# Performance work log

Measured on AMD Instinct MI355X. Metric: run time of the kernel, lower is better.

Reference implementation:

```python
import jax, jax.numpy as jnp
import numpy as np

N_HEAD, N_KV, HEAD_DIM, GATE_CH = 16, 4, 128, 32

def _rope(x, cos, sin):
    d = x.shape[3] // 2
    x1, x2 = x[..., :d], x[..., d:]
    return jnp.concatenate([x1 * cos + x2 * sin, x1 * (-sin) + x2 * cos], axis=3)

def _rmsnorm(x):
    xf = x.astype(jnp.float32)
    return (x * jax.lax.rsqrt(jnp.mean(xf * xf, axis=-1, keepdims=True) + 1e-6)).astype(x.dtype)

def setup_inputs() -> dict:
    key = jax.random.key(0)
    ks = jax.random.split(key, 9)
    B, T, C = 2, 2048, 2048
    return {
        "x":  jax.random.normal(ks[0], (B, T, C), jnp.float32),
        "ve": jax.random.normal(ks[1], (B, T, N_KV * HEAD_DIM), jnp.float32),
        "cos": jax.random.uniform(ks[2], (T, 1, HEAD_DIM // 2), jnp.float32),
        "sin": jax.random.uniform(ks[3], (T, 1, HEAD_DIM // 2), jnp.float32),
        "Wq": jax.random.normal(ks[4], (C, N_HEAD * HEAD_DIM), jnp.float32) * 0.02,
        "Wk": jax.random.normal(ks[5], (C, N_KV * HEAD_DIM), jnp.float32) * 0.02,
        "Wv": jax.random.normal(ks[6], (C, N_KV * HEAD_DIM), jnp.float32) * 0.02,
        "Wg": jax.random.normal(ks[7], (GATE_CH, N_KV), jnp.float32) * 0.02,
        "Wo": jax.random.normal(ks[8], (C, C), jnp.float32) * 0.02,
        "window": 1024,
    }

def reference(x, ve, cos, sin, Wq, Wk, Wv, Wg, Wo, window):
    B, T, C = x.shape
    q = (x @ Wq).reshape(B, T, N_HEAD, HEAD_DIM)
    k = (x @ Wk).reshape(B, T, N_KV, HEAD_DIM)
    v = (x @ Wv).reshape(B, T, N_KV, HEAD_DIM)
    # value-embedding gate (ve_gate active for this layer)
    gate = 2.0 * jax.nn.sigmoid(x[..., :GATE_CH] @ Wg)  # (B,T,N_KV)
    v = v + gate[..., None] * ve.reshape(B, T, N_KV, HEAD_DIM)
    q, k = _rope(q, cos, sin), _rope(k, cos, sin)
    q, k = _rmsnorm(q), _rmsnorm(k)
    # GQA: repeat kv heads (repeat_interleave over head dim)
    groups = N_HEAD // N_KV
    k = jnp.repeat(k, groups, axis=2)
    v = jnp.repeat(v, groups, axis=2)
    scale = 1.0 / np.sqrt(HEAD_DIM)
    scores = jnp.einsum("bthd,bshd->bhts", q, k) * scale  # (B,H,T,T)
    idx = jnp.arange(T)
    diff = idx[None, :] - idx[:, None]  # diff[i,j] = j - i, as in torch code
    mask = (diff >= 0) & (diff < window)
    scores = jnp.where(mask[None, None], scores, -jnp.inf)
    p = jax.nn.softmax(scores, axis=-1)
    y = jnp.einsum("bhts,bshd->bthd", p, v).reshape(B, T, C)
    return y @ Wo
```

## Files before the change

kernel.cpp:

```cpp
#include <hip/hip_runtime.h>
#include <hip/hip_bf16.h>
#include <cstdint>

typedef __hip_bfloat16 bf16;
typedef __attribute__((ext_vector_type(8))) short short8;
typedef __attribute__((ext_vector_type(4))) short short4v;
typedef __attribute__((ext_vector_type(4))) float f32x4;

#define T_   2048
#define CDIM 2048
#define NH   16
#define NKV  4
#define HD   128
#define QSCALE (0.08838834764831845f * 1.44269504088896340f)

__device__ __forceinline__ void gload_lds16(const void* g, void* l) {
  __builtin_amdgcn_global_load_lds(
      (const __attribute__((address_space(1))) void*)g,
      (__attribute__((address_space(3))) void*)l, 16, 0, 0);
}

__global__ __launch_bounds__(256) void cast_x_kernel(const float4* __restrict__ in,
                                                     ushort4* __restrict__ out, int n4) {
  int i = blockIdx.x * 256 + threadIdx.x;
  if (i >= n4) return;
  float4 v = in[i];
  union { bf16 h[4]; ushort4 u; } cv;
  cv.h[0] = __float2bfloat16(v.x);
  cv.h[1] = __float2bfloat16(v.y);
  cv.h[2] = __float2bfloat16(v.z);
  cv.h[3] = __float2bfloat16(v.w);
  out[i] = cv.u;
}

__global__ __launch_bounds__(256) void cast_transpose(const float* __restrict__ W,
                                                      bf16* __restrict__ WT,
                                                      int K, int N) {
  __shared__ float tile[32][33];
  int k0 = blockIdx.y * 32, n0 = blockIdx.x * 32;
  int r = threadIdx.x >> 5, c = threadIdx.x & 31;
  for (int i = 0; i < 4; ++i)
    tile[r + i * 8][c] = W[(size_t)(k0 + r + i * 8) * N + n0 + c];
  __syncthreads();
  for (int i = 0; i < 4; ++i)
    WT[(size_t)(n0 + r + i * 8) * K + k0 + c] = __float2bfloat16(tile[c][r + i * 8]);
}

__global__ __launch_bounds__(512, 2) void gemm_qkv8(const bf16* __restrict__ A,
                                                    const bf16* __restrict__ BT,
                                                    bf16* __restrict__ C,
                                                    int N, int K, int RY, int RX) {
  __shared__ __align__(16) bf16 sA[2][256 * 64];
  __shared__ __align__(16) bf16 sB[2][256 * 64];

  int tid = threadIdx.x;
  int lane = tid & 63, w = tid >> 6;
  int wm = w >> 2, wn = w & 3;
  int lr = lane & 15, lk = lane >> 4;

  int xcd = blockIdx.x & 7, t = blockIdx.x >> 3;
  int by = (xcd >> 1) * RY + t / RX;
  int bx = (xcd & 1) * RX + t % RX;
  int m0 = by * 256, n0 = bx * 256;

  f32x4 acc[8][4];
#pragma unroll
  for (int m = 0; m < 8; ++m)
#pragma unroll
    for (int n = 0; n < 4; ++n) acc[m][n] = (f32x4){0.f, 0.f, 0.f, 0.f};

  const bf16* Abase = A + (size_t)m0 * K;
  const bf16* Bbase = BT + (size_t)n0 * K;

  auto stageB = [&](int p, int kt) {
    int kb = kt << 6;
#pragma unroll
    for (int i = 0; i < 4; ++i) {
      int c = i * 512 + tid;
      int r = c >> 3, sl = c & 7;
      gload_lds16(Bbase + (size_t)r * K + kb + ((sl ^ (r & 7)) << 3),
                  (char*)(&sB[p][0]) + c * 16);
    }
  };
  auto stageAq = [&](int p, int kt, int q) {
    int kb = kt << 6;
    int rbase = 32 * q + ((w & 3) << 3) + ((w >> 2) << 7);
    int r = rbase + (lane >> 3), sl = lane & 7;
    gload_lds16(Abase + (size_t)r * K + kb + ((sl ^ (r & 7)) << 3),
                (char*)(&sA[p][0]) + rbase * 128 + lane * 16);
  };

  int nk = K >> 6;
  stageB(0, 0);
  stageAq(0, 0, 0); stageAq(0, 0, 1); stageAq(0, 0, 2); stageAq(0, 0, 3);
  stageB(1, 1);
  stageAq(1, 1, 0); stageAq(1, 1, 1); stageAq(1, 1, 2);
  asm volatile("s_waitcnt vmcnt(7)" ::: "memory");
  __builtin_amdgcn_s_barrier();

#define READ_A(Q)                                                          \
  {                                                                        \
    _Pragma("unroll")                                                      \
    for (int mi = 0; mi < 2; ++mi) {                                       \
      int row = wm * 128 + (2 * (Q) + mi) * 16 + lr;                       \
      const char* rb = sAb + row * 128;                                    \
      int rx = (row & 7) << 4;                                             \
      af[mi][0] = *(const short8*)(rb + ((lk * 16) ^ rx));                 \
      af[mi][1] = *(const short8*)(rb + ((64 + lk * 16) ^ rx));            \
    }                                                                      \
  }
#define MFMA_Q(Q)                                                          \
  __builtin_amdgcn_s_setprio(1);                                          \
  _Pragma("unroll")                                                        \
  for (int kk = 0; kk < 2; ++kk)                                           \
    _Pragma("unroll")                                                      \
    for (int mi = 0; mi < 2; ++mi)                                         \
      _Pragma("unroll")                                                    \
      for (int n = 0; n < 4; ++n)                                          \
        acc[2 * (Q) + mi][n] = __builtin_amdgcn_mfma_f32_16x16x32_bf16(    \
            af[mi][kk], bfr[n][kk], acc[2 * (Q) + mi][n], 0, 0, 0);        \
  __builtin_amdgcn_s_setprio(0);
#define LGKM_FENCE                                                         \
  asm volatile("s_waitcnt lgkmcnt(0)" ::: "memory");                       \
  __builtin_amdgcn_sched_barrier(0);

  for (int kt = 0; kt < nk; ++kt) {
    int p = kt & 1;
    const char* sAb = (const char*)(&sA[p][0]);
    const char* sBb = (const char*)(&sB[p][0]);
    short8 bfr[4][2], af[2][2];

#pragma unroll
    for (int n = 0; n < 4; ++n) {
      int row = wn * 64 + n * 16 + lr;
      const char* rb = sBb + row * 128;
      int rx = (row & 7) << 4;
      bfr[n][0] = *(const short8*)(rb + ((lk * 16) ^ rx));
      bfr[n][1] = *(const short8*)(rb + ((64 + lk * 16) ^ rx));
    }
    READ_A(0);
    if (kt + 1 < nk) stageAq(p ^ 1, kt + 1, 3);
    LGKM_FENCE;
    MFMA_Q(0);
    __builtin_amdgcn_s_barrier();

    READ_A(1);
    if (kt + 2 < nk) { stageB(p, kt + 2); stageAq(p, kt + 2, 0); }
    LGKM_FENCE;
    MFMA_Q(1);
    __builtin_amdgcn_s_barrier();

    READ_A(2);
    if (kt + 2 < nk) stageAq(p, kt + 2, 1);
    LGKM_FENCE;
    MFMA_Q(2);
    __builtin_amdgcn_s_barrier();

    READ_A(3);
    if (kt + 2 < nk) stageAq(p, kt + 2, 2);
    LGKM_FENCE;
    MFMA_Q(3);
    if (kt + 2 < nk)
      asm volatile("s_waitcnt vmcnt(7)" ::: "memory");
    else
      asm volatile("s_waitcnt vmcnt(0)" ::: "memory");
    __builtin_amdgcn_s_barrier();
  }
#undef READ_A
#undef MFMA_Q
#undef LGKM_FENCE

#pragma unroll
  for (int m = 0; m < 8; ++m)
#pragma unroll
    for (int n = 0; n < 4; ++n)
#pragma unroll
      for (int jj = 0; jj < 4; ++jj)
        C[(size_t)(m0 + wm * 128 + m * 16 + lk * 4 + jj) * N +
          n0 + wn * 64 + n * 16 + lr] = __float2bfloat16(acc[m][n][jj]);
}

template <int MREP, typename CT>
__global__ __launch_bounds__(512, 2) void gemm_8p(const bf16* __restrict__ A,
                                                  const bf16* __restrict__ BT,
                                                  CT* __restrict__ C,
                                                  int N, int K, int RY, int RX) {
  constexpr int BM = MREP * 32;
  constexpr int ALOADS = BM / 64;
  __shared__ __align__(16) bf16 sA[2][BM * 64];
  __shared__ __align__(16) bf16 sB[2][256 * 64];

  int tid = threadIdx.x;
  int lane = tid & 63, w = tid >> 6;
  int wm = w >> 2, wn = w & 3;
  int lr = lane & 15, lk = lane >> 4;

  int xcd = blockIdx.x & 7, t = blockIdx.x >> 3;
  int by = (xcd >> 1) * RY + t / RX;
  int bx = (xcd & 1) * RX + t % RX;
  int m0 = by * BM, n0 = bx * 256;

  f32x4 acc[MREP][4];
#pragma unroll
  for (int m = 0; m < MREP; ++m)
#pragma unroll
    for (int n = 0; n < 4; ++n) acc[m][n] = (f32x4){0.f, 0.f, 0.f, 0.f};

  const bf16* Abase = A + (size_t)m0 * K;
  const bf16* Bbase = BT + (size_t)n0 * K;

  auto stage = [&](int b, int kt) {
    int kb = kt << 6;
#pragma unroll
    for (int i = 0; i < ALOADS; ++i) {
      int c = i * 512 + tid;
      int r = c >> 3, sl = c & 7;
      gload_lds16(Abase + (size_t)r * K + kb + ((sl ^ (r & 7)) << 3),
                  (char*)(&sA[b][0]) + c * 16);
    }
#pragma unroll
    for (int i = 0; i < 4; ++i) {
      int c = i * 512 + tid;
      int r = c >> 3, sl = c & 7;
      gload_lds16(Bbase + (size_t)r * K + kb + ((sl ^ (r & 7)) << 3),
                  (char*)(&sB[b][0]) + c * 16);
    }
  };

  int nk = K >> 6;
  stage(0, 0);
  stage(1, 1);
  asm volatile("s_waitcnt vmcnt(6)" ::: "memory");
  __builtin_amdgcn_s_barrier();

  for (int kt = 0; kt < nk; ++kt) {
    int d = kt & 1;
    const char* sAb = (const char*)(&sA[d][0]);
    const char* sBb = (const char*)(&sB[d][0]);

    short8 bfr[4][2];
#pragma unroll
    for (int n = 0; n < 4; ++n) {
      int row = wn * 64 + n * 16 + lr;
      const char* rb = sBb + row * 128;
      int rx = (row & 7) << 4;
      bfr[n][0] = *(const short8*)(rb + ((lk * 16) ^ rx));
      bfr[n][1] = *(const short8*)(rb + ((64 + lk * 16) ^ rx));
    }

#pragma unroll
    for (int p = 0; p < MREP / 2; ++p) {
      short8 af[2][2];
#pragma unroll
      for (int mi = 0; mi < 2; ++mi) {
        int row = wm * (MREP * 16) + (p * 2 + mi) * 16 + lr;
        const char* rb = sAb + row * 128;
        int rx = (row & 7) << 4;
        af[mi][0] = *(const short8*)(rb + ((lk * 16) ^ rx));
        af[mi][1] = *(const short8*)(rb + ((64 + lk * 16) ^ rx));
      }
      __builtin_amdgcn_s_setprio(1);
#pragma unroll
      for (int kk = 0; kk < 2; ++kk)
#pragma unroll
        for (int mi = 0; mi < 2; ++mi)
#pragma unroll
          for (int n = 0; n < 4; ++n)
            acc[p * 2 + mi][n] = __builtin_amdgcn_mfma_f32_16x16x32_bf16(
                af[mi][kk], bfr[n][kk], acc[p * 2 + mi][n], 0, 0, 0);
      __builtin_amdgcn_s_setprio(0);
    }

    asm volatile("s_waitcnt lgkmcnt(0)\n\ts_barrier" ::: "memory");
    if (kt + 2 < nk) {
      stage(d, kt + 2);
      asm volatile("s_waitcnt vmcnt(6)\n\ts_barrier" ::: "memory");
    } else {
      asm volatile("s_waitcnt vmcnt(0)\n\ts_barrier" ::: "memory");
    }
  }

#pragma unroll
  for (int m = 0; m < MREP; ++m)
#pragma unroll
    for (int n = 0; n < 4; ++n)
#pragma unroll
      for (int jj = 0; jj < 4; ++jj) {
        size_t idx = (size_t)(m0 + wm * (MREP * 16) + m * 16 + lk * 4 + jj) * N +
                     n0 + wn * 64 + n * 16 + lr;
        if constexpr (__is_same(CT, float))
          C[idx] = acc[m][n][jj];
        else
          C[idx] = __float2bfloat16(acc[m][n][jj]);
      }
}

__global__ __launch_bounds__(256) void epilogue_kernel(
    const bf16* __restrict__ qkv, const float* __restrict__ x,
    const float* __restrict__ ve, const float* __restrict__ cosT,
    const float* __restrict__ sinT, const float* __restrict__ Wg,
    bf16* __restrict__ qn, bf16* __restrict__ kn, bf16* __restrict__ vT) {
  int row = blockIdx.x;
  int bi = row >> 11, t = row & 2047;
  int tid = threadIdx.x, lane = tid & 63, w = tid >> 6;
  __shared__ float gate[NKV];
  size_t rb = (size_t)row * 3072;

  if (tid < 128) {
    int g = tid >> 5, i = tid & 31;
    float p = x[(size_t)row * CDIM + i] * Wg[i * 4 + g];
    p += __shfl_xor(p, 1);  p += __shfl_xor(p, 2);
    p += __shfl_xor(p, 4);  p += __shfl_xor(p, 8);
    p += __shfl_xor(p, 16);
    if (i == 0) gate[g] = 2.f / (1.f + __expf(-p));
  }
  __syncthreads();

  float cv = cosT[t * 64 + lane];
  float sv = sinT[t * 64 + lane];

  for (int it = 0; it < 4; ++it) {
    int h = it * 4 + w;
    float x1 = __bfloat162float(qkv[rb + h * 128 + lane]);
    float x2 = __bfloat162float(qkv[rb + h * 128 + 64 + lane]);
    float y1 = x1 * cv + x2 * sv;
    float y2 = x2 * cv - x1 * sv;
    float ss = y1 * y1 + y2 * y2;
    ss += __shfl_xor(ss, 1);  ss += __shfl_xor(ss, 2);  ss += __shfl_xor(ss, 4);
    ss += __shfl_xor(ss, 8);  ss += __shfl_xor(ss, 16); ss += __shfl_xor(ss, 32);
    float r = rsqrtf(ss * (1.f / 128.f) + 1e-6f) * QSCALE;
    size_t ob = (size_t)row * (NH * HD) + h * 128;
    qn[ob + lane] = __float2bfloat16(y1 * r);
    qn[ob + 64 + lane] = __float2bfloat16(y2 * r);
  }
  {
    int h = w;
    float x1 = __bfloat162float(qkv[rb + 2048 + h * 128 + lane]);
    float x2 = __bfloat162float(qkv[rb + 2048 + h * 128 + 64 + lane]);
    float y1 = x1 * cv + x2 * sv;
    float y2 = x2 * cv - x1 * sv;
    float ss = y1 * y1 + y2 * y2;
    ss += __shfl_xor(ss, 1);  ss += __shfl_xor(ss, 2);  ss += __shfl_xor(ss, 4);
    ss += __shfl_xor(ss, 8);  ss += __shfl_xor(ss, 16); ss += __shfl_xor(ss, 32);
    float r = rsqrtf(ss * (1.f / 128.f) + 1e-6f);
    size_t ob = (size_t)row * (NKV * HD) + h * 128;
    kn[ob + lane] = __float2bfloat16(y1 * r);
    kn[ob + 64 + lane] = __float2bfloat16(y2 * r);
  }
  for (int e = tid; e < 512; e += 256) {
    int kv = e >> 7, d = e & 127;
    float val = __bfloat162float(qkv[rb + 2560 + e]) + gate[kv] * ve[(size_t)row * 512 + e];
    vT[((size_t)(bi * NKV + kv) * HD + d) * T_ + t] = __float2bfloat16(val);
  }
}

__global__ __launch_bounds__(256, 3) void attn_kernel(
    const bf16* __restrict__ qn, const bf16* __restrict__ kn,
    const bf16* __restrict__ vT, bf16* __restrict__ y,
    const int* __restrict__ winp) {
  __shared__ __align__(16) bf16 sK[64 * 128];
  __shared__ __align__(16) bf16 sV[128 * 64];

  int win = *winp;
  int id = blockIdx.x;
  int g  = id & 7;
  int bi = g >> 2, kvh = g & 3;
  int rem = id >> 3;
  int h  = kvh * 4 + (rem & 3);
  int jslot = (rem >> 2) & 7;
  int s5 = rem >> 5;
  int q0i = (s5 == 0) ? (2 * jslot) : (s5 == 1) ? (2 * jslot + 1)
          : (s5 == 2) ? (16 + jslot) : (31 - jslot);
  int q0 = q0i << 6;
  int tid = threadIdx.x;
  int lane = tid & 63, w = tid >> 6;
  int lr = lane & 15, lk = lane >> 4;

  short8 qf[4];
  {
    const bf16* qrow = qn + (size_t)(bi * T_ + q0 + w * 16 + lr) * (NH * HD) + h * HD;
#pragma unroll
    for (int c = 0; c < 4; ++c) qf[c] = *(const short8*)(qrow + c * 32 + lk * 8);
  }

  int kge[4], klb[4], vge[4], vlbA[4], vlbB[4];
#pragma unroll
  for (int i = 0; i < 4; ++i) {
    int c = i * 256 + tid;
    int kr = c >> 4, ks = c & 15;
    kge[i] = kr * (NKV * HD) + ks * 8;
    klb[i] = kr * 256 + ((ks ^ (kr & 7)) << 4);
    int vr = c >> 3, vs = c & 7;
    vge[i] = vr * T_ + vs * 8;
    int hh = vs >> 2, m = vs & 3, a = m >> 1;
    int sA = 8 * ((2 * m) & 3) + 4 * a;
    int sB = 8 * ((2 * m + 1) & 3) + 4 * a;
    int tA = 64 * hh + 2 * sA, tB = 64 * hh + 2 * sB;
    vlbA[i] = vr * 128 + (((tA >> 4) ^ (vr & 7)) << 4) + (tA & 15);
    vlbB[i] = vr * 128 + (((tB >> 4) ^ (vr & 7)) << 4) + (tB & 15);
  }
  const bf16* kpane = kn + (size_t)bi * T_ * (NKV * HD) + kvh * HD;
  const bf16* vpane = vT + (size_t)(bi * NKV + kvh) * HD * T_;

  short8 kreg[4], vreg[4];
  auto LOAD = [&](int jtx) {
    const bf16* kb = kpane + (size_t)(jtx << 6) * (NKV * HD);
    const bf16* vb = vpane + (jtx << 6);
#pragma unroll
    for (int i = 0; i < 4; ++i) kreg[i] = *(const short8*)(kb + kge[i]);
#pragma unroll
    for (int i = 0; i < 4; ++i) vreg[i] = *(const short8*)(vb + vge[i]);
  };
  auto WRITE = [&]() {
#pragma unroll
    for (int i = 0; i < 4; ++i) *(short8*)((char*)sK + klb[i]) = kreg[i];
#pragma unroll
    for (int i = 0; i < 4; ++i) {
      union { short8 s8; short4v s4[2]; } u;
      u.s8 = vreg[i];
      *(short4v*)((char*)sV + vlbA[i]) = u.s4[0];
      *(short4v*)((char*)sV + vlbB[i]) = u.s4[1];
    }
  };

  f32x4 o[8];
#pragma unroll
  for (int i = 0; i < 8; ++i) o[i] = (f32x4){0.f, 0.f, 0.f, 0.f};
  float lpart = 0.f;

  int jt0 = q0 >> 6;
  int hi = q0 + 62 + win; if (hi > T_ - 1) hi = T_ - 1;
  int jt1 = hi >> 6;

  LOAD(jt0);
  WRITE();
  if (jt0 < jt1) LOAD(jt0 + 1);
  asm volatile("s_waitcnt lgkmcnt(0)\n\ts_barrier" ::: "memory");

  int irow = q0 + w * 16 + lr;
  int klo = lk * 4;

  for (int jt = jt0; jt <= jt1; ++jt) {
    int j0 = jt << 6;

    f32x4 s[4];
#pragma unroll
    for (int sub = 0; sub < 4; ++sub) s[sub] = (f32x4){0.f, 0.f, 0.f, 0.f};
    __builtin_amdgcn_s_setprio(1);
#pragma unroll
    for (int sub = 0; sub < 4; ++sub) {
      int kr = sub * 16 + lr;
      int rx = (kr & 7) << 4;
      const char* rowb = (const char*)sK + kr * 256;
#pragma unroll
      for (int c = 0; c < 4; ++c) {
        short8 kf = *(const short8*)(rowb + ((c * 64 + lk * 16) ^ rx));
        s[sub] = __builtin_amdgcn_mfma_f32_16x16x32_bf16(kf, qf[c], s[sub], 0, 0, 0);
      }
    }
    __builtin_amdgcn_s_setprio(0);

    bool full = (j0 >= q0 + 64) && (j0 + 64 <= q0 + win);
    int koff = j0 - irow;

    unsigned pk[8];
#pragma unroll
    for (int sub = 0; sub < 4; ++sub) {
      float p0 = exp2f(s[sub][0]), p1 = exp2f(s[sub][1]);
      float p2 = exp2f(s[sub][2]), p3 = exp2f(s[sub][3]);
      if (!full) {
        int base = koff + sub * 16 + klo;
        p0 = ((unsigned)(base + 0) < (unsigned)win) ? p0 : 0.f;
        p1 = ((unsigned)(base + 1) < (unsigned)win) ? p1 : 0.f;
        p2 = ((unsigned)(base + 2) < (unsigned)win) ? p2 : 0.f;
        p3 = ((unsigned)(base + 3) < (unsigned)win) ? p3 : 0.f;
      }
      lpart += (p0 + p1) + (p2 + p3);
      asm("v_cvt_pk_bf16_f32 %0, %1, %2" : "=v"(pk[sub * 2])     : "v"(p0), "v"(p1));
      asm("v_cvt_pk_bf16_f32 %0, %1, %2" : "=v"(pk[sub * 2 + 1]) : "v"(p2), "v"(p3));
    }
    union { unsigned u[4]; short8 s8; } c0, c1;
    c0.u[0] = pk[0]; c0.u[1] = pk[1]; c0.u[2] = pk[2]; c0.u[3] = pk[3];
    c1.u[0] = pk[4]; c1.u[1] = pk[5]; c1.u[2] = pk[6]; c1.u[3] = pk[7];
    short8 pf0 = c0.s8, pf1 = c1.s8;

    __builtin_amdgcn_s_setprio(1);
#pragma unroll
    for (int nb = 0; nb < 8; ++nb) {
      int vr = nb * 16 + lr;
      int vrx = (vr & 7) << 4;
      const char* vb = (const char*)sV + vr * 128;
      short8 vf0 = *(const short8*)(vb + ((lk * 16) ^ vrx));
      short8 vf1 = *(const short8*)(vb + ((64 + lk * 16) ^ vrx));
      o[nb] = __builtin_amdgcn_mfma_f32_16x16x32_bf16(pf0, vf0, o[nb], 0, 0, 0);
      o[nb] = __builtin_amdgcn_mfma_f32_16x16x32_bf16(pf1, vf1, o[nb], 0, 0, 0);
    }
    __builtin_amdgcn_s_setprio(0);

    asm volatile("s_waitcnt lgkmcnt(0)\n\ts_barrier" ::: "memory");
    if (jt < jt1) {
      WRITE();
      if (jt + 1 < jt1) LOAD(jt + 2);
      asm volatile("s_waitcnt lgkmcnt(0)\n\ts_barrier" ::: "memory");
    }
  }

  float l = lpart;
  l += __shfl_xor(l, 16);
  l += __shfl_xor(l, 32);
#pragma unroll
  for (int jj = 0; jj < 4; ++jj) {
    float inv = 1.f / __shfl(l, klo + jj);
    size_t ob = (size_t)(bi * T_ + q0 + w * 16 + klo + jj) * (NH * HD) + h * HD;
#pragma unroll
    for (int nb = 0; nb < 8; ++nb)
      y[ob + nb * 16 + lr] = __float2bfloat16(o[nb][jj] * inv);
  }
}

extern "C" void kernel_launch(void* const* d_in, const int* in_sizes, int n_in,
                              void* d_out, int out_size, void* d_ws, size_t ws_size,
                              hipStream_t stream) {
  const float* x    = (const float*)d_in[0];
  const float* ve   = (const float*)d_in[1];
  const float* cosT = (const float*)d_in[2];
  const float* sinT = (const float*)d_in[3];
  const float* Wq   = (const float*)d_in[4];
  const float* Wk   = (const float*)d_in[5];
  const float* Wv   = (const float*)d_in[6];
  const float* Wg   = (const float*)d_in[7];
  const float* Wo   = (const float*)d_in[8];
  const int*   win  = (const int*)d_in[9];
  float* out = (float*)d_out;

  char* ws = (char*)d_ws;
  bf16*  xb   = (bf16*)(ws);
  bf16*  wT   = (bf16*)(ws + 16777216);
  bf16*  woT  = (bf16*)(ws + 29360128);
  bf16*  qkvb = (bf16*)(ws + 37748736);
  bf16*  qn   = (bf16*)(ws + 62914560);
  bf16*  kn   = (bf16*)(ws + 79691776);
  bf16*  vTb  = (bf16*)(ws + 83886080);
  bf16*  y    = qkvb;

  cast_x_kernel<<<8192, 256, 0, stream>>>((const float4*)x, (ushort4*)xb, 2097152);
  cast_transpose<<<dim3(64, 64), 256, 0, stream>>>(Wq, wT, 2048, 2048);
  cast_transpose<<<dim3(16, 64), 256, 0, stream>>>(Wk, wT + (size_t)2048 * 2048, 2048, 512);
  cast_transpose<<<dim3(16, 64), 256, 0, stream>>>(Wv, wT + (size_t)2560 * 2048, 2048, 512);
  cast_transpose<<<dim3(64, 64), 256, 0, stream>>>(Wo, woT, 2048, 2048);

  gemm_qkv8<<<192, 512, 0, stream>>>(xb, wT, qkvb, 3072, 2048, 4, 6);
  epilogue_kernel<<<4096, 256, 0, stream>>>(qkvb, x, ve, cosT, sinT, Wg, qn, kn, vTb);
  attn_kernel<<<1024, 256, 0, stream>>>(qn, kn, vTb, y, win);
  gemm_8p<4, float><<<256, 512, 0, stream>>>(y, woT, out, 2048, 2048, 8, 4);
}
```

Before: 200.9 us.

## Unify GEMMs into phased template; retile QKV GEMM to fill all CUs

Replaces the two GEMM kernels with one template, gemm_pp, parameterized by M and N repeat counts. It uses the phased pipeline in which A-tile loads are interleaved across four MFMA phases. The QKV projection now uses 256x192 tiles, giving a 256-block grid instead of 192 blocks, so every CU gets work. The output projection moves from the simpler double-buffered loop to the phased schedule, with vmcnt gates adjusted to the new number of loads in flight. Narrower N tiles lower per-block arithmetic intensity, and the new wait counts must match the load count exactly to stay correct.

```diff
diff --git a/kernel.cpp b/kernel.cpp
--- a/kernel.cpp
+++ b/kernel.cpp
@@ -18,6 +18,12 @@
   __builtin_amdgcn_global_load_lds(
       (const __attribute__((address_space(1))) void*)g,
       (__attribute__((address_space(3))) void*)l, 16, 0, 0);
+}
+
+template <int G> __device__ __forceinline__ void vm_gate() {
+  if constexpr (G == 6)      asm volatile("s_waitcnt vmcnt(6)" ::: "memory");
+  else if constexpr (G == 5) asm volatile("s_waitcnt vmcnt(5)" ::: "memory");
+  else                       asm volatile("s_waitcnt vmcnt(0)" ::: "memory");
 }
 
 __global__ __launch_bounds__(256) void cast_x_kernel(const float4* __restrict__ in,
@@ -46,12 +52,18 @@
     WT[(size_t)(n0 + r + i * 8) * K + k0 + c] = __float2bfloat16(tile[c][r + i * 8]);
 }
 
-__global__ __launch_bounds__(512, 2) void gemm_qkv8(const bf16* __restrict__ A,
-                                                    const bf16* __restrict__ BT,
-                                                    bf16* __restrict__ C,
-                                                    int N, int K, int RY, int RX) {
-  __shared__ __align__(16) bf16 sA[2][256 * 64];
-  __shared__ __align__(16) bf16 sB[2][256 * 64];
+template <int MREP, int NREP, typename CT>
+__global__ __launch_bounds__(512, 2) void gemm_pp(const bf16* __restrict__ A,
+                                                  const bf16* __restrict__ BT,
+                                                  CT* __restrict__ C,
+                                                  int N, int K, int RY, int RX) {
+  constexpr int BM = MREP * 32;
+  constexpr int BN = NREP * 64;
+  constexpr int QN = (MREP == 8) ? 4 : 2;
+  constexpr int MI = MREP / 4;
+  constexpr int GATE = NREP + QN - 1;
+  __shared__ __align__(16) bf16 sA[2][BM * 64];
+  __shared__ __align__(16) bf16 sB[2][BN * 64];
 
   int tid = threadIdx.x;
   int lane = tid & 63, w = tid >> 6;
@@ -61,13 +73,13 @@
   int xcd = blockIdx.x & 7, t = blockIdx.x >> 3;
   int by = (xcd >> 1) * RY + t / RX;
   int bx = (xcd & 1) * RX + t % RX;
-  int m0 = by * 256, n0 = bx * 256;
-
-  f32x4 acc[8][4];
-#pragma unroll
-  for (int m = 0; m < 8; ++m)
-#pragma unroll
-    for (int n = 0; n < 4; ++n) acc[m][n] = (f32x4){0.f, 0.f, 0.f, 0.f};
+  int m0 = by * BM, n0 = bx * BN;
+
+  f32x4 acc[MREP][NREP];
+#pragma unroll
+  for (int m = 0; m < MREP; ++m)
+#pragma unroll
+    for (int n = 0; n < NREP; ++n) acc[m][n] = (f32x4){0.f, 0.f, 0.f, 0.f};
 
   const bf16* Abase = A + (size_t)m0 * K;
   const bf16* Bbase = BT + (size_t)n0 * K;
@@ -75,7 +87,7 @@
   auto stageB = [&](int p, int kt) {
     int kb = kt << 6;
 #pragma unroll
-    for (int i = 0; i < 4; ++i) {
+    for (int i = 0; i < NREP; ++i) {
       int c = i * 512 + tid;
       int r = c >> 3, sl = c & 7;
       gload_lds16(Bbase + (size_t)r * K + kb + ((sl ^ (r & 7)) << 3),
@@ -84,7 +96,7 @@
   };
   auto stageAq = [&](int p, int kt, int q) {
     int kb = kt << 6;
-    int rbase = 32 * q + ((w & 3) << 3) + ((w >> 2) << 7);
+    int rbase = 32 * q + ((w & 3) << 3) + ((w >> 2) * (BM / 2));
     int r = rbase + (lane >> 3), sl = lane & 7;
     gload_lds16(Abase + (size_t)r * K + kb + ((sl ^ (r & 7)) << 3),
                 (char*)(&sA[p][0]) + rbase * 128 + lane * 16);
@@ -92,33 +104,35 @@
 
   int nk = K >> 6;
   stageB(0, 0);
-  stageAq(0, 0, 0); stageAq(0, 0, 1); stageAq(0, 0, 2); stageAq(0, 0, 3);
+#pragma unroll
+  for (int q = 0; q < QN; ++q) stageAq(0, 0, q);
   stageB(1, 1);
-  stageAq(1, 1, 0); stageAq(1, 1, 1); stageAq(1, 1, 2);
-  asm volatile("s_waitcnt vmcnt(7)" ::: "memory");
+#pragma unroll
+  for (int q = 0; q < QN - 1; ++q) stageAq(1, 1, q);
+  vm_gate<GATE>();
   __builtin_amdgcn_s_barrier();
 
-#define READ_A(Q)                                                          \
+#define READ_A_FRAGS(PH)                                                   \
   {                                                                        \
     _Pragma("unroll")                                                      \
-    for (int mi = 0; mi < 2; ++mi) {                                       \
-      int row = wm * 128 + (2 * (Q) + mi) * 16 + lr;                       \
+    for (int mi = 0; mi < MI; ++mi) {                                      \
+      int row = wm * (MREP * 16) + ((PH) * MI + mi) * 16 + lr;             \
       const char* rb = sAb + row * 128;                                    \
       int rx = (row & 7) << 4;                                             \
       af[mi][0] = *(const short8*)(rb + ((lk * 16) ^ rx));                 \
       af[mi][1] = *(const short8*)(rb + ((64 + lk * 16) ^ rx));            \
     }                                                                      \
   }
-#define MFMA_Q(Q)                                                          \
-  __builtin_amdgcn_s_setprio(1);                                          \
+#define MFMA_PH(PH)                                                        \
+  __builtin_amdgcn_s_setprio(1);                                           \
   _Pragma("unroll")                                                        \
   for (int kk = 0; kk < 2; ++kk)                                           \
     _Pragma("unroll")                                                      \
-    for (int mi = 0; mi < 2; ++mi)                                         \
+    for (int mi = 0; mi < MI; ++mi)                                        \
       _Pragma("unroll")                                                    \
-      for (int n = 0; n < 4; ++n)                                          \
-        acc[2 * (Q) + mi][n] = __builtin_amdgcn_mfma_f32_16x16x32_bf16(    \
-            af[mi][kk], bfr[n][kk], acc[2 * (Q) + mi][n], 0, 0, 0);        \
+      for (int n = 0; n < NREP; ++n)                                       \
+        acc[(PH) * MI + mi][n] = __builtin_amdgcn_mfma_f32_16x16x32_bf16(  \
+            af[mi][kk], bfr[n][kk], acc[(PH) * MI + mi][n], 0, 0, 0);      \
   __builtin_amdgcn_s_setprio(0);
 #define LGKM_FENCE                                                         \
   asm volatile("s_waitcnt lgkmcnt(0)" ::: "memory");                       \
@@ -128,166 +142,59 @@
     int p = kt & 1;
     const char* sAb = (const char*)(&sA[p][0]);
     const char* sBb = (const char*)(&sB[p][0]);
-    short8 bfr[4][2], af[2][2];
-
-#pragma unroll
-    for (int n = 0; n < 4; ++n) {
-      int row = wn * 64 + n * 16 + lr;
+    short8 bfr[NREP][2], af[MI][2];
+
+#pragma unroll
+    for (int n = 0; n < NREP; ++n) {
+      int row = wn * (NREP * 16) + n * 16 + lr;
       const char* rb = sBb + row * 128;
       int rx = (row & 7) << 4;
       bfr[n][0] = *(const short8*)(rb + ((lk * 16) ^ rx));
       bfr[n][1] = *(const short8*)(rb + ((64 + lk * 16) ^ rx));
     }
-    READ_A(0);
-    if (kt + 1 < nk) stageAq(p ^ 1, kt + 1, 3);
+    READ_A_FRAGS(0);
+    if (kt + 1 < nk) stageAq(p ^ 1, kt + 1, QN - 1);
     LGKM_FENCE;
-    MFMA_Q(0);
+    MFMA_PH(0);
     __builtin_amdgcn_s_barrier();
 
-    READ_A(1);
-    if (kt + 2 < nk) { stageB(p, kt + 2); stageAq(p, kt + 2, 0); }
+    READ_A_FRAGS(1);
+    if (kt + 2 < nk) {
+      stageB(p, kt + 2);
+      if constexpr (QN == 4) stageAq(p, kt + 2, 0);
+    }
     LGKM_FENCE;
-    MFMA_Q(1);
+    MFMA_PH(1);
     __builtin_amdgcn_s_barrier();
 
-    READ_A(2);
-    if (kt + 2 < nk) stageAq(p, kt + 2, 1);
+    READ_A_FRAGS(2);
+    if (kt + 2 < nk) stageAq(p, kt + 2, (QN == 4) ? 1 : 0);
     LGKM_FENCE;
-    MFMA_Q(2);
+    MFMA_PH(2);
     __builtin_amdgcn_s_barrier();
 
-    READ_A(3);
-    if (kt + 2 < nk) stageAq(p, kt + 2, 2);
+    READ_A_FRAGS(3);
+    if constexpr (QN == 4) {
+      if (kt + 2 < nk) stageAq(p, kt + 2, 2);
+    }
     LGKM_FENCE;
-    MFMA_Q(3);
-    if (kt + 2 < nk)
-      asm volatile("s_waitcnt vmcnt(7)" ::: "memory");
-    else
-      asm volatile("s_waitcnt vmcnt(0)" ::: "memory");
+    MFMA_PH(3);
+    if (kt + 2 < nk) vm_gate<GATE>();
+    else             vm_gate<0>();
     __builtin_amdgcn_s_barrier();
   }
-#undef READ_A
-#undef MFMA_Q
+#undef READ_A_FRAGS
+#undef MFMA_PH
 #undef LGKM_FENCE
 
 #pragma unroll
-  for (int m = 0; m < 8; ++m)
-#pragma unroll
-    for (int n = 0; n < 4; ++n)
-#pragma unroll
-      for (int jj = 0; jj < 4; ++jj)
-        C[(size_t)(m0 + wm * 128 + m * 16 + lk * 4 + jj) * N +
-          n0 + wn * 64 + n * 16 + lr] = __float2bfloat16(acc[m][n][jj]);
-}
-
-template <int MREP, typename CT>
-__global__ __launch_bounds__(512, 2) void gemm_8p(const bf16* __restrict__ A,
-                                                  const bf16* __restrict__ BT,
-                                                  CT* __restrict__ C,
-                                                  int N, int K, int RY, int RX) {
-  constexpr int BM = MREP * 32;
-  constexpr int ALOADS = BM / 64;
-  __shared__ __align__(16) bf16 sA[2][BM * 64];
-  __shared__ __align__(16) bf16 sB[2][256 * 64];
-
-  int tid = threadIdx.x;
-  int lane = tid & 63, w = tid >> 6;
-  int wm = w >> 2, wn = w & 3;
-  int lr = lane & 15, lk = lane >> 4;
-
-  int xcd = blockIdx.x & 7, t = blockIdx.x >> 3;
-  int by = (xcd >> 1) * RY + t / RX;
-  int bx = (xcd & 1) * RX + t % RX;
-  int m0 = by * BM, n0 = bx * 256;
-
-  f32x4 acc[MREP][4];
-#pragma unroll
   for (int m = 0; m < MREP; ++m)
 #pragma unroll
-    for (int n = 0; n < 4; ++n) acc[m][n] = (f32x4){0.f, 0.f, 0.f, 0.f};
-
-  const bf16* Abase = A + (size_t)m0 * K;
-  const bf16* Bbase = BT + (size_t)n0 * K;
-
-  auto stage = [&](int b, int kt) {
-    int kb = kt << 6;
-#pragma unroll
-    for (int i = 0; i < ALOADS; ++i) {
-      int c = i * 512 + tid;
-      int r = c >> 3, sl = c & 7;
-      gload_lds16(Abase + (size_t)r * K + kb + ((sl ^ (r & 7)) << 3),
-                  (char*)(&sA[b][0]) + c * 16);
-    }
-#pragma unroll
-    for (int i = 0; i < 4; ++i) {
-      int c = i * 512 + tid;
-      int r = c >> 3, sl = c & 7;
-      gload_lds16(Bbase + (size_t)r * K + kb + ((sl ^ (r & 7)) << 3),
-                  (char*)(&sB[b][0]) + c * 16);
-    }
-  };
-
-  int nk = K >> 6;
-  stage(0, 0);
-  stage(1, 1);
-  asm volatile("s_waitcnt vmcnt(6)" ::: "memory");
-  __builtin_amdgcn_s_barrier();
-
-  for (int kt = 0; kt < nk; ++kt) {
-    int d = kt & 1;
-    const char* sAb = (const char*)(&sA[d][0]);
-    const char* sBb = (const char*)(&sB[d][0]);
-
-    short8 bfr[4][2];
-#pragma unroll
-    for (int n = 0; n < 4; ++n) {
-      int row = wn * 64 + n * 16 + lr;
-      const char* rb = sBb + row * 128;
-      int rx = (row & 7) << 4;
-      bfr[n][0] = *(const short8*)(rb + ((lk * 16) ^ rx));
-      bfr[n][1] = *(const short8*)(rb + ((64 + lk * 16) ^ rx));
-    }
-
-#pragma unroll
-    for (int p = 0; p < MREP / 2; ++p) {
-      short8 af[2][2];
-#pragma unroll
-      for (int mi = 0; mi < 2; ++mi) {
-        int row = wm * (MREP * 16) + (p * 2 + mi) * 16 + lr;
-        const char* rb = sAb + row * 128;
-        int rx = (row & 7) << 4;
-        af[mi][0] = *(const short8*)(rb + ((lk * 16) ^ rx));
-        af[mi][1] = *(const short8*)(rb + ((64 + lk * 16) ^ rx));
-      }
-      __builtin_amdgcn_s_setprio(1);
-#pragma unroll
-      for (int kk = 0; kk < 2; ++kk)
-#pragma unroll
-        for (int mi = 0; mi < 2; ++mi)
-#pragma unroll
-          for (int n = 0; n < 4; ++n)
-            acc[p * 2 + mi][n] = __builtin_amdgcn_mfma_f32_16x16x32_bf16(
-                af[mi][kk], bfr[n][kk], acc[p * 2 + mi][n], 0, 0, 0);
-      __builtin_amdgcn_s_setprio(0);
-    }
-
-    asm volatile("s_waitcnt lgkmcnt(0)\n\ts_barrier" ::: "memory");
-    if (kt + 2 < nk) {
-      stage(d, kt + 2);
-      asm volatile("s_waitcnt vmcnt(6)\n\ts_barrier" ::: "memory");
-    } else {
-      asm volatile("s_waitcnt vmcnt(0)\n\ts_barrier" ::: "memory");
-    }
-  }
-
-#pragma unroll
-  for (int m = 0; m < MREP; ++m)
-#pragma unroll
-    for (int n = 0; n < 4; ++n)
+    for (int n = 0; n < NREP; ++n)
 #pragma unroll
       for (int jj = 0; jj < 4; ++jj) {
         size_t idx = (size_t)(m0 + wm * (MREP * 16) + m * 16 + lk * 4 + jj) * N +
-                     n0 + wn * 64 + n * 16 + lr;
+                     n0 + wn * (NREP * 16) + n * 16 + lr;
         if constexpr (__is_same(CT, float))
           C[idx] = acc[m][n][jj];
         else
@@ -549,8 +456,8 @@
   cast_transpose<<<dim3(16, 64), 256, 0, stream>>>(Wv, wT + (size_t)2560 * 2048, 2048, 512);
   cast_transpose<<<dim3(64, 64), 256, 0, stream>>>(Wo, woT, 2048, 2048);
 
-  gemm_qkv8<<<192, 512, 0, stream>>>(xb, wT, qkvb, 3072, 2048, 4, 6);
+  gemm_pp<8, 3, bf16><<<256, 512, 0, stream>>>(xb, wT, qkvb, 3072, 2048, 4, 8);
   epilogue_kernel<<<4096, 256, 0, stream>>>(qkvb, x, ve, cosT, sinT, Wg, qn, kn, vTb);
   attn_kernel<<<1024, 256, 0, stream>>>(qn, kn, vTb, y, win);
-  gemm_8p<4, float><<<256, 512, 0, stream>>>(y, woT, out, 2048, 2048, 8, 4);
-}
+  gemm_pp<4, 4, float><<<256, 512, 0, stream>>>(y, woT, out, 2048, 2048, 8, 4);
+}
```

Result: no change. 198.1 us (-1.4%).
